# Optimization experiments

Hardware: AMD Instinct MI355X
Metric: run time of the kernel (lower is better)

## Reference

```python
import jax, jax.numpy as jnp
import numpy as np

H, DK, DV = 4, 64, 64        # heads, key/value head dims (hidden=256)
M, TOPK = 4, 2               # num memories, router top-k
GN, EPS, COND_SCALE = 16.0, 1e-5, 1.0


def setup_inputs() -> dict:
    key = jax.random.key(0)
    ks = jax.random.split(key, 12)
    B, Q, K, D = 8, 64, 256, 256
    w = lambda k, shape, fan: jax.random.normal(k, shape, jnp.float32) / np.sqrt(fan).astype(np.float32)
    return {
        "query": jax.random.normal(ks[0], (B, Q, D), jnp.float32),
        "keyval": jax.random.normal(ks[1], (B, K, D), jnp.float32),
        "attention_mask_kv": jnp.ones((B, K), jnp.int32),
        "W_cond": w(ks[2], (D, D), D),
        "W_q": w(ks[3], (D, H * DK), D),
        "W_k": w(ks[4], (D, H * DK), D),
        "W_v": w(ks[5], (D, H * DV), D),
        "W_gk1": w(ks[6], (D, 16), D),
        "W_gk2": w(ks[7], (16, H * DK), 16),
        "b_gk2": jnp.zeros((H * DK,), jnp.float32),
        "W_router": w(ks[8], (D, M), D),
        "norm_w": jnp.ones((DV,), jnp.float32),
        "W_o": w(ks[9], (H * DV, D), H * DV),
    }


def _mem_last(q_last, k, v, gk, sel, wgt):
    """Last-token output of one gated linear-attention memory.
    S_t = diag(exp(gk_t)) S_{t-1} + k_t v_t^T ; o_T = q_T S_T.
    q_last: (N,H,DK); k,gk: (N,K,H,DK); v: (N,K,H,DV); sel,wgt: (N,K)."""
    k_e = k * sel[:, :, None, None]
    v_e = v * wgt[:, :, None, None]
    gk_e = gk * sel[:, :, None, None]          # unselected tokens: no decay, no update
    G = jnp.cumsum(gk_e, axis=1)               # (N,K,H,DK), log decays
    decay = jnp.exp(G[:, -1:, :, :] - G)       # remaining decay to last step, <= 1
    s = jnp.einsum('nhd,nthd->nth', q_last, k_e * decay)
    return jnp.einsum('nth,nthv->nhv', s, v_e)


def reference(query, keyval, attention_mask_kv, W_cond, W_q, W_k, W_v,
              W_gk1, W_gk2, b_gk2, W_router, norm_w, W_o):
    B, Q, D = query.shape
    K = keyval.shape[1]
    N = B * Q
    # broadcast KV expansion + cond injection
    cond = (query @ W_cond) * COND_SCALE                         # (B,Q,D)
    x = (keyval[:, None, :, :] + cond[:, :, None, :]).reshape(N, K, D)
    m = jnp.broadcast_to(attention_mask_kv[:, None, :].astype(x.dtype), (B, Q, K)).reshape(N, K)
    # projections
    q = (x @ W_q).reshape(N, K, H, DK)
    k = (x @ W_k).reshape(N, K, H, DK) * m[:, :, None, None]
    v = (x @ W_v).reshape(N, K, H, DV) * m[:, :, None, None]
    gk = (jax.nn.log_sigmoid(x @ W_gk1 @ W_gk2 + b_gk2) / GN).reshape(N, K, H, DK)
    gk = gk * m[:, :, None, None]
    # router: softmax -> top-k -> renormalize
    router_logits = (x @ W_router).reshape(N * K, M)
    probs = jax.nn.softmax(router_logits, axis=-1)
    topv, topi = jax.lax.top_k(probs, TOPK)
    topv = topv / jnp.sum(topv, axis=-1, keepdims=True)
    w_mem = jnp.sum(jax.nn.one_hot(topi, M, dtype=x.dtype) * topv[..., None], axis=-2)
    w_mem = w_mem.reshape(N, K, M)
    # shared memory (always on) + routed memories
    q_last = q[:, -1]
    ones = jnp.ones((N, K), x.dtype)
    o = _mem_last(q_last, k, v, gk, ones, ones)
    for e in range(M):
        we = w_mem[:, :, e]
        o = o + _mem_last(q_last, k, v, gk, (we > 0).astype(x.dtype), we)
    # per-head RMSNorm + output projection
    o = o * jax.lax.rsqrt(jnp.mean(o * o, axis=-1, keepdims=True) + EPS) * norm_w
    out = (o.reshape(N, H * DV) @ W_o).reshape(B, Q, D)
    return out, router_logits
```

## Files before the change

kernel.cpp:

```cpp
#include <hip/hip_runtime.h>
#include <math.h>

#define Bb   8
#define Qq   64
#define Kk   256
#define Dd   256
#define Nn   (Bb * Qq)
#define GNi  0.0625f
#define EPSf 1e-5f
#define WB   1088

__device__ __forceinline__ float wred(float x) {
#pragma unroll
    for (int off = 32; off > 0; off >>= 1)
        x += __shfl_xor(x, off, 64);
    return x;
}

__global__ __launch_bounds__(256) void pack_wb(
    const float* __restrict__ Wq, const float* __restrict__ Wk,
    const float* __restrict__ Wv, const float* __restrict__ Wg1,
    const float* __restrict__ Wg2, const float* __restrict__ Wr,
    float* __restrict__ Wb)
{
    const int idx = blockIdx.x * 256 + threadIdx.x;
    const int k = idx / WB, j = idx % WB;
    float v;
    if (j < 256)       v = Wq[(size_t)k * 256 + j];
    else if (j < 512)  v = Wk[(size_t)k * 256 + j - 256];
    else if (j < 768)  v = Wv[(size_t)k * 256 + j - 512];
    else if (j < 1024) {
        const int c = j - 768;
        float s = 0.f;
#pragma unroll
        for (int i = 0; i < 16; ++i)
            s = fmaf(Wg1[(size_t)k * 16 + i], Wg2[(size_t)i * 256 + c], s);
        v = s;
    }
    else if (j < 1028) v = Wr[(size_t)k * 4 + (j - 1024)];
    else               v = 0.f;
    Wb[idx] = v;
}

__device__ __forceinline__ void gemm_core(
    const float* __restrict__ A, const float* __restrict__ Bm, int ldb,
    float (&acc)[8][4], float* As, float* Ws)
{
    const int tid = threadIdx.x;
    const int r  = tid >> 1;
    const int kl = (tid & 1) * 8;
    const int wc = tid & 63;
    const int kr = (tid >> 6) * 4;
    const int ty = tid >> 4;
    const int tx = tid & 15;

    for (int k0 = 0; k0 < Dd; k0 += 16) {
        const float4 a0 = *(const float4*)(A + (size_t)r * Dd + k0 + kl);
        const float4 a1 = *(const float4*)(A + (size_t)r * Dd + k0 + kl + 4);
        As[(kl + 0) * 132 + r] = a0.x;
        As[(kl + 1) * 132 + r] = a0.y;
        As[(kl + 2) * 132 + r] = a0.z;
        As[(kl + 3) * 132 + r] = a0.w;
        As[(kl + 4) * 132 + r] = a1.x;
        As[(kl + 5) * 132 + r] = a1.y;
        As[(kl + 6) * 132 + r] = a1.z;
        As[(kl + 7) * 132 + r] = a1.w;
#pragma unroll
        for (int u = 0; u < 4; ++u)
            Ws[(kr + u) * 68 + wc] = Bm[(size_t)(k0 + kr + u) * ldb + wc];
        __syncthreads();
#pragma unroll
        for (int kk = 0; kk < 16; ++kk) {
            const float4 aL = *(const float4*)&As[kk * 132 + ty * 8];
            const float4 aH = *(const float4*)&As[kk * 132 + ty * 8 + 4];
            const float4 bv = *(const float4*)&Ws[kk * 68 + tx * 4];
            const float av[8] = {aL.x, aL.y, aL.z, aL.w, aH.x, aH.y, aH.z, aH.w};
            const float bw[4] = {bv.x, bv.y, bv.z, bv.w};
#pragma unroll
            for (int i = 0; i < 8; ++i)
#pragma unroll
                for (int j = 0; j < 4; ++j)
                    acc[i][j] = fmaf(av[i], bw[j], acc[i][j]);
        }
        __syncthreads();
    }
}

__global__ __launch_bounds__(256) void gemm1(
    const float* __restrict__ keyval, const float* __restrict__ query,
    const float* __restrict__ Wb, const float* __restrict__ W_cond,
    float* __restrict__ KVi, float* __restrict__ KVr,
    float* __restrict__ cond, float* __restrict__ KVq8)
{
    __shared__ float As[16 * 132];
    __shared__ float Ws[16 * 68];
    const int id = blockIdx.x;
    const int tid = threadIdx.x;

    if (id == 224) {
        for (int b8 = 0; b8 < 8; ++b8)
            As[b8 * 256 + tid] = keyval[((size_t)b8 * Kk + 255) * Dd + tid];
        __syncthreads();
        float acc8[8] = {};
        for (int k = 0; k < 256; ++k) {
            const float wq = Wb[(size_t)k * WB + tid];
#pragma unroll
            for (int b8 = 0; b8 < 8; ++b8)
                acc8[b8] = fmaf(As[b8 * 256 + k], wq, acc8[b8]);
        }
        for (int b8 = 0; b8 < 8; ++b8)
            KVq8[b8 * 256 + tid] = acc8[b8];
        return;
    }

    float acc[8][4] = {};
    const int ty = tid >> 4, tx = tid & 15;

    if (id < 208) {
        const int bm  = (id / 13) * 128;
        const int bnA = 256 + (id % 13) * 64;
        gemm_core(keyval + (size_t)bm * Dd, Wb + bnA, WB, acc, As, Ws);
        if (bnA < 1024) {
            const int reg = (bnA >> 8) - 1;
            const int cb  = bnA & 255;
#pragma unroll
            for (int i = 0; i < 8; ++i) {
                const size_t rowo = (size_t)(bm + ty * 8 + i) * 1024;
#pragma unroll
                for (int jj = 0; jj < 4; ++jj)
                    KVi[rowo + (size_t)(cb + tx * 4 + jj) * 4 + reg] = acc[i][jj];
            }
        } else if (tx == 0) {
#pragma unroll
            for (int i = 0; i < 8; ++i)
                *(float4*)&KVr[(size_t)(bm + ty * 8 + i) * 4] =
                    make_float4(acc[i][0], acc[i][1], acc[i][2], acc[i][3]);
        }
    } else {
        const int id2 = id - 208;
        const int bm = (id2 >> 2) * 128;
        const int bn = (id2 & 3) * 64;
        gemm_core(query + (size_t)bm * Dd, W_cond + bn, Dd, acc, As, Ws);
#pragma unroll
        for (int i = 0; i < 8; ++i)
            *(float4*)&cond[(size_t)(bm + ty * 8 + i) * Dd + bn + tx * 4] =
                make_float4(acc[i][0], acc[i][1], acc[i][2], acc[i][3]);
    }
}

__global__ __launch_bounds__(256) void gemm2(
    const float* __restrict__ cond, const float* __restrict__ Wb,
    float* __restrict__ Cbi, float* __restrict__ Cr)
{
    __shared__ float As[16 * 132];
    __shared__ float Ws[16 * 68];
    const int id = blockIdx.x;
    const int tid = threadIdx.x;
    const int bm = (id / 17) * 128;
    const int bn = (id % 17) * 64;
    float acc[8][4] = {};
    gemm_core(cond + (size_t)bm * Dd, Wb + bn, WB, acc, As, Ws);
    const int ty = tid >> 4, tx = tid & 15;
    if (bn < 1024) {
        const int reg = bn >> 8;
        const int cb  = bn & 255;
#pragma unroll
        for (int i = 0; i < 8; ++i) {
            const size_t rowo = (size_t)(bm + ty * 8 + i) * 1024;
#pragma unroll
            for (int jj = 0; jj < 4; ++jj)
                Cbi[rowo + (size_t)(cb + tx * 4 + jj) * 4 + reg] = acc[i][jj];
        }
    } else if (tx == 0) {
#pragma unroll
        for (int i = 0; i < 8; ++i)
            *(float4*)&Cr[(size_t)(bm + ty * 8 + i) * 4] =
                make_float4(acc[i][0], acc[i][1], acc[i][2], acc[i][3]);
    }
}

__device__ __forceinline__ void tile_step(
    const float4* buf, int t0, const int* __restrict__ pm, const float4* wm,
    float ql, float kc, float vc, float pc,
    float& E0, float& E1, float& E2, float& E3, float& E4, float& o,
    float (*Pt)[68], float* sb, int lane, int tl, int qq)
{
    float vreg[16];
#pragma unroll
    for (int i = 0; i < 16; ++i) {
        const int t = t0 + 15 - i;
        const float mf = (float)pm[t];
        const float4 kv = buf[i];
        const float kkv = (kv.x + kc) * mf;
        vreg[i] = (kv.y + vc) * mf;
        const float pre = kv.z + pc;
        const float4 w = wm[t];
        const float ls = fminf(pre, 0.f) - __logf(1.f + __expf(-fabsf(pre)));
        float dg = __expf(ls * GNi);
        dg = (mf != 0.f) ? dg : 1.f;
        const float zf = E0 + w.x * E1 + w.y * E2 + w.z * E3 + w.w * E4;
        Pt[i][lane] = ql * kkv * zf;
        E0 *= dg;
        E1 *= (w.x > 0.f) ? dg : 1.f;
        E2 *= (w.y > 0.f) ? dg : 1.f;
        E3 *= (w.z > 0.f) ? dg : 1.f;
        E4 *= (w.w > 0.f) ? dg : 1.f;
    }
    __builtin_amdgcn_wave_barrier();
    float s = 0.f;
#pragma unroll
    for (int r = 0; r < 4; ++r) {
        const float4 p4 = *(const float4*)&Pt[tl][qq * 16 + r * 4];
        s += (p4.x + p4.y) + (p4.z + p4.w);
    }
    s += __shfl_xor(s, 16, 64);
    s += __shfl_xor(s, 32, 64);
    sb[tl] = s;
    __builtin_amdgcn_wave_barrier();
#pragma unroll
    for (int r = 0; r < 4; ++r) {
        const float4 sv = *(const float4*)&sb[r * 4];
        o = fmaf(sv.x, vreg[r * 4 + 0], o);
        o = fmaf(sv.y, vreg[r * 4 + 1], o);
        o = fmaf(sv.z, vreg[r * 4 + 2], o);
        o = fmaf(sv.w, vreg[r * 4 + 3], o);
    }
}

__global__ __launch_bounds__(256, 2) void mom_fused(
    const float4* __restrict__ KVi, const float* __restrict__ KVr,
    const float4* __restrict__ Cbi, const float* __restrict__ Cr,
    const float* __restrict__ KVq8, const float* __restrict__ b_gk2,
    const int* __restrict__ mask, const float* __restrict__ W_o,
    const float* __restrict__ norm_w,
    float* __restrict__ out, float* __restrict__ logits)
{
    __shared__ float4 wm[Kk];
    __shared__ float  Ptile[4][16][68];
    __shared__ float  sbuf[4][16];
    __shared__ float  onorm[Dd];

    const int n = blockIdx.x;
    const int b = n >> 6;
    const int j = threadIdx.x;
    const int lane = j & 63;
    const int wv = j >> 6;

    const float4 c4 = Cbi[(size_t)n * 256 + j];
    const float qc = c4.x, kc = c4.y, vc = c4.z;
    const float pc = c4.w + b_gk2[j];
    const float ql = KVq8[b * 256 + j] + qc;

    {
        const float4 kvr = *(const float4*)&KVr[(size_t)(b * Kk + j) * 4];
        const float4 cr  = *(const float4*)&Cr[(size_t)n * 4];
        float l[4] = {kvr.x + cr.x, kvr.y + cr.y, kvr.z + cr.z, kvr.w + cr.w};
        *(float4*)(logits + ((size_t)n * Kk + j) * 4) =
            make_float4(l[0], l[1], l[2], l[3]);

        int i1 = 0;
#pragma unroll
        for (int q = 1; q < 4; ++q) if (l[q] > l[i1]) i1 = q;
        int i2 = -1;
#pragma unroll
        for (int q = 0; q < 4; ++q) {
            if (q == i1) continue;
            if (i2 < 0 || l[q] > l[i2]) i2 = q;
        }
        const float mx = fmaxf(l[i1], l[i2]);
        const float e1 = __expf(l[i1] - mx);
        const float e2 = __expf(l[i2] - mx);
        const float inv = 1.f / (e1 + e2);
        float w[4] = {0.f, 0.f, 0.f, 0.f};
        w[i1] = e1 * inv;
        w[i2] = e2 * inv;
        wm[j] = make_float4(w[0], w[1], w[2], w[3]);
    }
    __syncthreads();

    const float4* pkv = KVi + (size_t)b * Kk * 256 + j;
    const int*    pm  = mask + b * Kk;

    float E0 = 1.f, E1 = 1.f, E2 = 1.f, E3 = 1.f, E4 = 1.f;
    float o = 0.f;
    const int tl = lane & 15, qq = lane >> 4;

    float4 bufA[16], bufB[16];
#pragma unroll
    for (int i = 0; i < 16; ++i) bufA[i] = pkv[(size_t)(255 - i) * 256];

    for (int pp = 0; pp < 8; ++pp) {
        const int tA = 240 - 32 * pp;
        const int tB = tA - 16;
#pragma unroll
        for (int i = 0; i < 16; ++i) bufB[i] = pkv[(size_t)(tB + 15 - i) * 256];
        tile_step(bufA, tA, pm, wm, ql, kc, vc, pc,
                  E0, E1, E2, E3, E4, o, Ptile[wv], sbuf[wv], lane, tl, qq);
        if (pp < 7) {
#pragma unroll
            for (int i = 0; i < 16; ++i)
                bufA[i] = pkv[(size_t)(tB - 16 + 15 - i) * 256];
        }
        tile_step(bufB, tB, pm, wm, ql, kc, vc, pc,
                  E0, E1, E2, E3, E4, o, Ptile[wv], sbuf[wv], lane, tl, qq);
    }

    const float ms = wred(o * o) * (1.0f / 64.0f);
    onorm[j] = o * rsqrtf(ms + EPSf) * norm_w[lane];
    __syncthreads();

    float acc = 0.f;
#pragma unroll 8
    for (int k = 0; k < Dd; ++k)
        acc = fmaf(onorm[k], W_o[(size_t)k * Dd + j], acc);
    out[(size_t)n * Dd + j] = acc;
}

extern "C" void kernel_launch(void* const* d_in, const int* in_sizes, int n_in,
                              void* d_out, int out_size, void* d_ws, size_t ws_size,
                              hipStream_t stream)
{
    const float* query    = (const float*)d_in[0];
    const float* keyval   = (const float*)d_in[1];
    const int*   mask     = (const int*)  d_in[2];
    const float* W_cond   = (const float*)d_in[3];
    const float* W_q      = (const float*)d_in[4];
    const float* W_k      = (const float*)d_in[5];
    const float* W_v      = (const float*)d_in[6];
    const float* W_gk1    = (const float*)d_in[7];
    const float* W_gk2    = (const float*)d_in[8];
    const float* b_gk2    = (const float*)d_in[9];
    const float* W_router = (const float*)d_in[10];
    const float* norm_w   = (const float*)d_in[11];
    const float* W_o      = (const float*)d_in[12];

    float* out    = (float*)d_out;
    float* logits = out + Nn * Dd;

    float* p = (float*)d_ws;
    float* Wb   = p; p += Dd * WB;
    float* KVi  = p; p += (size_t)Bb * Kk * 1024;
    float* KVr  = p; p += Bb * Kk * 4;
    float* cond = p; p += Nn * Dd;
    float* Cbi  = p; p += (size_t)Nn * 1024;
    float* Cr   = p; p += Nn * 4;
    float* KVq8 = p; p += Bb * Dd;

    pack_wb<<<(Dd * WB) / 256, dim3(256), 0, stream>>>(
        W_q, W_k, W_v, W_gk1, W_gk2, W_router, Wb);

    gemm1<<<225, dim3(256), 0, stream>>>(
        keyval, query, Wb, W_cond, KVi, KVr, cond, KVq8);

    gemm2<<<68, dim3(256), 0, stream>>>(cond, Wb, Cbi, Cr);

    mom_fused<<<Nn, dim3(256), 0, stream>>>(
        (const float4*)KVi, KVr, (const float4*)Cbi, Cr,
        KVq8, b_gk2, mask, W_o, norm_w, out, logits);
}
```

Before: 208.0 us.

## Restructure projection GEMMs, shrink recurrence tile, swizzle blocks across XCDs

Drops the weight-packing kernel and replaces the two GEMM kernels with a prep kernel and a main GEMM. The main GEMM uses a 64x64 tile with register prefetch, computes several projections against one shared A tile, and writes the interleaved k/v/g layout with float4 stores. The router projections become simple per-element dot products. In the fused recurrence kernel, the time tile shrinks from 16 to 8 steps, the mask is staged in LDS, and the block-to-row mapping is swizzled so each batch's KV data stays on one XCD's L2. The risks are more barrier and reduction rounds per time step and lower reuse in the smaller GEMM tiles.

```diff
diff --git a/kernel.cpp b/kernel.cpp
--- a/kernel.cpp
+++ b/kernel.cpp
@@ -8,7 +8,6 @@
 #define Nn   (Bb * Qq)
 #define GNi  0.0625f
 #define EPSf 1e-5f
-#define WB   1088
 
 __device__ __forceinline__ float wred(float x) {
 #pragma unroll
@@ -17,179 +16,183 @@
     return x;
 }
 
-__global__ __launch_bounds__(256) void pack_wb(
-    const float* __restrict__ Wq, const float* __restrict__ Wk,
-    const float* __restrict__ Wv, const float* __restrict__ Wg1,
+template<int R>
+__device__ __forceinline__ void gemm64(
+    const float* __restrict__ A, int lda,
+    const float* __restrict__ B0, const float* __restrict__ B1,
+    const float* __restrict__ B2, const float* __restrict__ B3,
+    int bn, int Kc, float (&acc)[R][16], float* As, float* Ws)
+{
+    const int tid = threadIdx.x;
+    const int aRow = tid >> 2, aCol = (tid & 3) * 4;
+    const int wr = tid >> 4, wcb = (tid & 15) * 4;
+    const int ty = tid >> 4, tx = tid & 15;
+    const float* Bp[4] = {B0, B1, B2, B3};
+
+    float4 rA = *(const float4*)(A + (size_t)aRow * lda + aCol);
+    float4 rW[R];
+#pragma unroll
+    for (int r = 0; r < R; ++r)
+        rW[r] = *(const float4*)(Bp[r] + (size_t)wr * 256 + bn + wcb);
+
+    for (int k0 = 0; k0 < Kc; k0 += 16) {
+        __syncthreads();
+        As[(aCol + 0) * 68 + aRow] = rA.x;
+        As[(aCol + 1) * 68 + aRow] = rA.y;
+        As[(aCol + 2) * 68 + aRow] = rA.z;
+        As[(aCol + 3) * 68 + aRow] = rA.w;
+#pragma unroll
+        for (int r = 0; r < R; ++r)
+            *(float4*)&Ws[r * 1088 + wr * 68 + wcb] = rW[r];
+        __syncthreads();
+        if (k0 + 16 < Kc) {
+            rA = *(const float4*)(A + (size_t)aRow * lda + k0 + 16 + aCol);
+#pragma unroll
+            for (int r = 0; r < R; ++r)
+                rW[r] = *(const float4*)(Bp[r] + (size_t)(k0 + 16 + wr) * 256 + bn + wcb);
+        }
+#pragma unroll
+        for (int kk = 0; kk < 16; ++kk) {
+            const float4 a4 = *(const float4*)&As[kk * 68 + ty * 4];
+            const float av[4] = {a4.x, a4.y, a4.z, a4.w};
+#pragma unroll
+            for (int r = 0; r < R; ++r) {
+                const float4 b4 = *(const float4*)&Ws[r * 1088 + kk * 68 + tx * 4];
+                const float bw[4] = {b4.x, b4.y, b4.z, b4.w};
+#pragma unroll
+                for (int i = 0; i < 4; ++i)
+#pragma unroll
+                    for (int j = 0; j < 4; ++j)
+                        acc[r][i * 4 + j] = fmaf(av[i], bw[j], acc[r][i * 4 + j]);
+            }
+        }
+    }
+}
+
+__global__ __launch_bounds__(256) void prep(
+    const float* __restrict__ query, const float* __restrict__ keyval,
+    const float* __restrict__ W_cond, const float* __restrict__ Wg1,
     const float* __restrict__ Wg2, const float* __restrict__ Wr,
-    float* __restrict__ Wb)
-{
-    const int idx = blockIdx.x * 256 + threadIdx.x;
-    const int k = idx / WB, j = idx % WB;
-    float v;
-    if (j < 256)       v = Wq[(size_t)k * 256 + j];
-    else if (j < 512)  v = Wk[(size_t)k * 256 + j - 256];
-    else if (j < 768)  v = Wv[(size_t)k * 256 + j - 512];
-    else if (j < 1024) {
-        const int c = j - 768;
-        float s = 0.f;
-#pragma unroll
-        for (int i = 0; i < 16; ++i)
-            s = fmaf(Wg1[(size_t)k * 16 + i], Wg2[(size_t)i * 256 + c], s);
-        v = s;
-    }
-    else if (j < 1028) v = Wr[(size_t)k * 4 + (j - 1024)];
-    else               v = 0.f;
-    Wb[idx] = v;
-}
-
-__device__ __forceinline__ void gemm_core(
-    const float* __restrict__ A, const float* __restrict__ Bm, int ldb,
-    float (&acc)[8][4], float* As, float* Ws)
-{
-    const int tid = threadIdx.x;
-    const int r  = tid >> 1;
-    const int kl = (tid & 1) * 8;
-    const int wc = tid & 63;
-    const int kr = (tid >> 6) * 4;
-    const int ty = tid >> 4;
-    const int tx = tid & 15;
-
-    for (int k0 = 0; k0 < Dd; k0 += 16) {
-        const float4 a0 = *(const float4*)(A + (size_t)r * Dd + k0 + kl);
-        const float4 a1 = *(const float4*)(A + (size_t)r * Dd + k0 + kl + 4);
-        As[(kl + 0) * 132 + r] = a0.x;
-        As[(kl + 1) * 132 + r] = a0.y;
-        As[(kl + 2) * 132 + r] = a0.z;
-        As[(kl + 3) * 132 + r] = a0.w;
-        As[(kl + 4) * 132 + r] = a1.x;
-        As[(kl + 5) * 132 + r] = a1.y;
-        As[(kl + 6) * 132 + r] = a1.z;
-        As[(kl + 7) * 132 + r] = a1.w;
-#pragma unroll
-        for (int u = 0; u < 4; ++u)
-            Ws[(kr + u) * 68 + wc] = Bm[(size_t)(k0 + kr + u) * ldb + wc];
-        __syncthreads();
-#pragma unroll
-        for (int kk = 0; kk < 16; ++kk) {
-            const float4 aL = *(const float4*)&As[kk * 132 + ty * 8];
-            const float4 aH = *(const float4*)&As[kk * 132 + ty * 8 + 4];
-            const float4 bv = *(const float4*)&Ws[kk * 68 + tx * 4];
-            const float av[8] = {aL.x, aL.y, aL.z, aL.w, aH.x, aH.y, aH.z, aH.w};
-            const float bw[4] = {bv.x, bv.y, bv.z, bv.w};
-#pragma unroll
-            for (int i = 0; i < 8; ++i)
-#pragma unroll
-                for (int j = 0; j < 4; ++j)
-                    acc[i][j] = fmaf(av[i], bw[j], acc[i][j]);
-        }
-        __syncthreads();
-    }
-}
-
-__global__ __launch_bounds__(256) void gemm1(
-    const float* __restrict__ keyval, const float* __restrict__ query,
-    const float* __restrict__ Wb, const float* __restrict__ W_cond,
-    float* __restrict__ KVi, float* __restrict__ KVr,
-    float* __restrict__ cond, float* __restrict__ KVq8)
-{
-    __shared__ float As[16 * 132];
-    __shared__ float Ws[16 * 68];
+    const float* __restrict__ Wq,
+    float* __restrict__ cond, float* __restrict__ Wg,
+    float* __restrict__ KVr, float* __restrict__ KVq8)
+{
+    __shared__ float lds[2 * 1088];
     const int id = blockIdx.x;
     const int tid = threadIdx.x;
 
-    if (id == 224) {
+    if (id < 48) {
+        float acc[1][16] = {};
+        const int ty = tid >> 4, tx = tid & 15;
+        if (id < 32) {
+            const int bm = (id >> 2) * 64, bn = (id & 3) * 64;
+            gemm64<1>(query + (size_t)bm * Dd, Dd, W_cond, nullptr, nullptr, nullptr,
+                      bn, Dd, acc, lds, lds + 1088);
+#pragma unroll
+            for (int i = 0; i < 4; ++i)
+                *(float4*)&cond[(size_t)(bm + ty * 4 + i) * Dd + bn + tx * 4] =
+                    make_float4(acc[0][i * 4 + 0], acc[0][i * 4 + 1],
+                                acc[0][i * 4 + 2], acc[0][i * 4 + 3]);
+        } else {
+            const int id3 = id - 32;
+            const int bm = (id3 >> 2) * 64, bn = (id3 & 3) * 64;
+            gemm64<1>(Wg1 + (size_t)bm * 16, 16, Wg2, nullptr, nullptr, nullptr,
+                      bn, 16, acc, lds, lds + 1088);
+#pragma unroll
+            for (int i = 0; i < 4; ++i)
+                *(float4*)&Wg[(size_t)(bm + ty * 4 + i) * Dd + bn + tx * 4] =
+                    make_float4(acc[0][i * 4 + 0], acc[0][i * 4 + 1],
+                                acc[0][i * 4 + 2], acc[0][i * 4 + 3]);
+        }
+        return;
+    }
+    if (id < 80) {
+        const int idx = (id - 48) * 256 + tid;
+        const int row = idx >> 2, col = idx & 3;
+        float a = 0.f;
+        for (int k = 0; k < 256; ++k)
+            a = fmaf(keyval[(size_t)row * Dd + k], Wr[(size_t)k * 4 + col], a);
+        KVr[idx] = a;
+        return;
+    }
+    for (int b8 = 0; b8 < 8; ++b8)
+        lds[b8 * 256 + tid] = keyval[((size_t)b8 * Kk + 255) * Dd + tid];
+    __syncthreads();
+    float a8[8] = {};
+    for (int k = 0; k < 256; ++k) {
+        const float wq = Wq[(size_t)k * Dd + tid];
+#pragma unroll
         for (int b8 = 0; b8 < 8; ++b8)
-            As[b8 * 256 + tid] = keyval[((size_t)b8 * Kk + 255) * Dd + tid];
-        __syncthreads();
-        float acc8[8] = {};
-        for (int k = 0; k < 256; ++k) {
-            const float wq = Wb[(size_t)k * WB + tid];
-#pragma unroll
-            for (int b8 = 0; b8 < 8; ++b8)
-                acc8[b8] = fmaf(As[b8 * 256 + k], wq, acc8[b8]);
-        }
-        for (int b8 = 0; b8 < 8; ++b8)
-            KVq8[b8 * 256 + tid] = acc8[b8];
-        return;
-    }
-
-    float acc[8][4] = {};
-    const int ty = tid >> 4, tx = tid & 15;
-
-    if (id < 208) {
-        const int bm  = (id / 13) * 128;
-        const int bnA = 256 + (id % 13) * 64;
-        gemm_core(keyval + (size_t)bm * Dd, Wb + bnA, WB, acc, As, Ws);
-        if (bnA < 1024) {
-            const int reg = (bnA >> 8) - 1;
-            const int cb  = bnA & 255;
-#pragma unroll
-            for (int i = 0; i < 8; ++i) {
-                const size_t rowo = (size_t)(bm + ty * 8 + i) * 1024;
-#pragma unroll
-                for (int jj = 0; jj < 4; ++jj)
-                    KVi[rowo + (size_t)(cb + tx * 4 + jj) * 4 + reg] = acc[i][jj];
-            }
-        } else if (tx == 0) {
-#pragma unroll
-            for (int i = 0; i < 8; ++i)
-                *(float4*)&KVr[(size_t)(bm + ty * 8 + i) * 4] =
-                    make_float4(acc[i][0], acc[i][1], acc[i][2], acc[i][3]);
-        }
-    } else {
-        const int id2 = id - 208;
-        const int bm = (id2 >> 2) * 128;
-        const int bn = (id2 & 3) * 64;
-        gemm_core(query + (size_t)bm * Dd, W_cond + bn, Dd, acc, As, Ws);
-#pragma unroll
-        for (int i = 0; i < 8; ++i)
-            *(float4*)&cond[(size_t)(bm + ty * 8 + i) * Dd + bn + tx * 4] =
-                make_float4(acc[i][0], acc[i][1], acc[i][2], acc[i][3]);
-    }
-}
-
-__global__ __launch_bounds__(256) void gemm2(
-    const float* __restrict__ cond, const float* __restrict__ Wb,
-    float* __restrict__ Cbi, float* __restrict__ Cr)
-{
-    __shared__ float As[16 * 132];
-    __shared__ float Ws[16 * 68];
+            a8[b8] = fmaf(lds[b8 * 256 + k], wq, a8[b8]);
+    }
+    for (int b8 = 0; b8 < 8; ++b8)
+        KVq8[b8 * 256 + tid] = a8[b8];
+}
+
+__global__ __launch_bounds__(256) void maingemm(
+    const float* __restrict__ keyval, const float* __restrict__ cond,
+    const float* __restrict__ Wq, const float* __restrict__ Wk,
+    const float* __restrict__ Wv, const float* __restrict__ Wg,
+    const float* __restrict__ Wr,
+    float* __restrict__ KVi, float* __restrict__ Cbi, float* __restrict__ Cr)
+{
+    __shared__ float lds[5 * 1088];
     const int id = blockIdx.x;
     const int tid = threadIdx.x;
-    const int bm = (id / 17) * 128;
-    const int bn = (id % 17) * 64;
-    float acc[8][4] = {};
-    gemm_core(cond + (size_t)bm * Dd, Wb + bn, WB, acc, As, Ws);
     const int ty = tid >> 4, tx = tid & 15;
-    if (bn < 1024) {
-        const int reg = bn >> 8;
-        const int cb  = bn & 255;
-#pragma unroll
-        for (int i = 0; i < 8; ++i) {
-            const size_t rowo = (size_t)(bm + ty * 8 + i) * 1024;
-#pragma unroll
-            for (int jj = 0; jj < 4; ++jj)
-                Cbi[rowo + (size_t)(cb + tx * 4 + jj) * 4 + reg] = acc[i][jj];
-        }
-    } else if (tx == 0) {
-#pragma unroll
-        for (int i = 0; i < 8; ++i)
-            *(float4*)&Cr[(size_t)(bm + ty * 8 + i) * 4] =
-                make_float4(acc[i][0], acc[i][1], acc[i][2], acc[i][3]);
-    }
-}
-
-__device__ __forceinline__ void tile_step(
-    const float4* buf, int t0, const int* __restrict__ pm, const float4* wm,
+
+    if (id < 128) {
+        const int bm = (id >> 2) * 64;
+        const int bn = (id & 3) * 64;
+        float acc[3][16] = {};
+        gemm64<3>(keyval + (size_t)bm * Dd, Dd, Wk, Wv, Wg, nullptr,
+                  bn, Dd, acc, lds, lds + 1088);
+#pragma unroll
+        for (int i = 0; i < 4; ++i) {
+            const size_t rowo = (size_t)(bm + ty * 4 + i) * 1024;
+#pragma unroll
+            for (int j = 0; j < 4; ++j)
+                *(float4*)&KVi[rowo + (size_t)(bn + tx * 4 + j) * 4] =
+                    make_float4(acc[0][i * 4 + j], acc[1][i * 4 + j],
+                                acc[2][i * 4 + j], 0.f);
+        }
+    } else if (id < 160) {
+        const int id2 = id - 128;
+        const int bm = (id2 >> 2) * 64;
+        const int bn = (id2 & 3) * 64;
+        float acc[4][16] = {};
+        gemm64<4>(cond + (size_t)bm * Dd, Dd, Wq, Wk, Wv, Wg,
+                  bn, Dd, acc, lds, lds + 1088);
+#pragma unroll
+        for (int i = 0; i < 4; ++i) {
+            const size_t rowo = (size_t)(bm + ty * 4 + i) * 1024;
+#pragma unroll
+            for (int j = 0; j < 4; ++j)
+                *(float4*)&Cbi[rowo + (size_t)(bn + tx * 4 + j) * 4] =
+                    make_float4(acc[0][i * 4 + j], acc[1][i * 4 + j],
+                                acc[2][i * 4 + j], acc[3][i * 4 + j]);
+        }
+    } else {
+        const int idx = (id - 160) * 256 + tid;
+        const int row = idx >> 2, col = idx & 3;
+        float a = 0.f;
+        for (int k = 0; k < 256; ++k)
+            a = fmaf(cond[(size_t)row * Dd + k], Wr[(size_t)k * 4 + col], a);
+        Cr[idx] = a;
+    }
+}
+
+__device__ __forceinline__ void tile_step8(
+    const float4* buf, int thi, const float* mfs, const float4* wm,
     float ql, float kc, float vc, float pc,
     float& E0, float& E1, float& E2, float& E3, float& E4, float& o,
     float (*Pt)[68], float* sb, int lane, int tl, int qq)
 {
-    float vreg[16];
-#pragma unroll
-    for (int i = 0; i < 16; ++i) {
-        const int t = t0 + 15 - i;
-        const float mf = (float)pm[t];
+    float vreg[8];
+#pragma unroll
+    for (int i = 0; i < 8; ++i) {
+        const int t = thi - i;
+        const float mf = mfs[t];
         const float4 kv = buf[i];
         const float kkv = (kv.x + kc) * mf;
         vreg[i] = (kv.y + vc) * mf;
@@ -198,7 +201,7 @@
         const float ls = fminf(pre, 0.f) - __logf(1.f + __expf(-fabsf(pre)));
         float dg = __expf(ls * GNi);
         dg = (mf != 0.f) ? dg : 1.f;
-        const float zf = E0 + w.x * E1 + w.y * E2 + w.z * E3 + w.w * E4;
+        const float zf = (E0 + w.x * E1) + (w.y * E2 + w.z * E3) + w.w * E4;
         Pt[i][lane] = ql * kkv * zf;
         E0 *= dg;
         E1 *= (w.x > 0.f) ? dg : 1.f;
@@ -207,24 +210,20 @@
         E4 *= (w.w > 0.f) ? dg : 1.f;
     }
     __builtin_amdgcn_wave_barrier();
-    float s = 0.f;
-#pragma unroll
-    for (int r = 0; r < 4; ++r) {
-        const float4 p4 = *(const float4*)&Pt[tl][qq * 16 + r * 4];
-        s += (p4.x + p4.y) + (p4.z + p4.w);
-    }
+    const float4 p0 = *(const float4*)&Pt[tl][qq * 8];
+    const float4 p1 = *(const float4*)&Pt[tl][qq * 8 + 4];
+    float s = ((p0.x + p0.y) + (p0.z + p0.w)) + ((p1.x + p1.y) + (p1.z + p1.w));
+    s += __shfl_xor(s, 8, 64);
     s += __shfl_xor(s, 16, 64);
     s += __shfl_xor(s, 32, 64);
     sb[tl] = s;
     __builtin_amdgcn_wave_barrier();
-#pragma unroll
-    for (int r = 0; r < 4; ++r) {
-        const float4 sv = *(const float4*)&sb[r * 4];
-        o = fmaf(sv.x, vreg[r * 4 + 0], o);
-        o = fmaf(sv.y, vreg[r * 4 + 1], o);
-        o = fmaf(sv.z, vreg[r * 4 + 2], o);
-        o = fmaf(sv.w, vreg[r * 4 + 3], o);
-    }
+    const float4 s0 = *(const float4*)&sb[0];
+    const float4 s1 = *(const float4*)&sb[4];
+    o = fmaf(s0.x, vreg[0], o); o = fmaf(s0.y, vreg[1], o);
+    o = fmaf(s0.z, vreg[2], o); o = fmaf(s0.w, vreg[3], o);
+    o = fmaf(s1.x, vreg[4], o); o = fmaf(s1.y, vreg[5], o);
+    o = fmaf(s1.z, vreg[6], o); o = fmaf(s1.w, vreg[7], o);
 }
 
 __global__ __launch_bounds__(256, 2) void mom_fused(
@@ -235,13 +234,15 @@
     const float* __restrict__ norm_w,
     float* __restrict__ out, float* __restrict__ logits)
 {
-    __shared__ float4 wm[Kk];
-    __shared__ float  Ptile[4][16][68];
-    __shared__ float  sbuf[4][16];
-    __shared__ float  onorm[Dd];
-
-    const int n = blockIdx.x;
-    const int b = n >> 6;
+    __shared__ __align__(16) float4 wm[Kk];
+    __shared__ __align__(16) float  mfs[Kk];
+    __shared__ __align__(16) float  Ptile[4][8][68];
+    __shared__ __align__(16) float  sbuf[4][8];
+    __shared__ __align__(16) float  onorm[Dd];
+
+    const int bi = blockIdx.x;
+    const int n = (bi & 7) * 64 + (bi >> 3);
+    const int b = bi & 7;
     const int j = threadIdx.x;
     const int lane = j & 63;
     const int wv = j >> 6;
@@ -252,6 +253,7 @@
     const float ql = KVq8[b * 256 + j] + qc;
 
     {
+        mfs[j] = (float)mask[b * Kk + j];
         const float4 kvr = *(const float4*)&KVr[(size_t)(b * Kk + j) * 4];
         const float4 cr  = *(const float4*)&Cr[(size_t)n * 4];
         float l[4] = {kvr.x + cr.x, kvr.y + cr.y, kvr.z + cr.z, kvr.w + cr.w};
@@ -279,30 +281,28 @@
     __syncthreads();
 
     const float4* pkv = KVi + (size_t)b * Kk * 256 + j;
-    const int*    pm  = mask + b * Kk;
 
     float E0 = 1.f, E1 = 1.f, E2 = 1.f, E3 = 1.f, E4 = 1.f;
     float o = 0.f;
-    const int tl = lane & 15, qq = lane >> 4;
-
-    float4 bufA[16], bufB[16];
-#pragma unroll
-    for (int i = 0; i < 16; ++i) bufA[i] = pkv[(size_t)(255 - i) * 256];
-
-    for (int pp = 0; pp < 8; ++pp) {
-        const int tA = 240 - 32 * pp;
-        const int tB = tA - 16;
-#pragma unroll
-        for (int i = 0; i < 16; ++i) bufB[i] = pkv[(size_t)(tB + 15 - i) * 256];
-        tile_step(bufA, tA, pm, wm, ql, kc, vc, pc,
-                  E0, E1, E2, E3, E4, o, Ptile[wv], sbuf[wv], lane, tl, qq);
-        if (pp < 7) {
-#pragma unroll
-            for (int i = 0; i < 16; ++i)
-                bufA[i] = pkv[(size_t)(tB - 16 + 15 - i) * 256];
-        }
-        tile_step(bufB, tB, pm, wm, ql, kc, vc, pc,
-                  E0, E1, E2, E3, E4, o, Ptile[wv], sbuf[wv], lane, tl, qq);
+    const int tl = lane & 7, qq = lane >> 3;
+
+    float4 bufA[8], bufB[8];
+#pragma unroll
+    for (int i = 0; i < 8; ++i) bufA[i] = pkv[(size_t)(255 - i) * 256];
+
+    for (int p = 0; p < 16; ++p) {
+        const int tA = 255 - 16 * p;
+        const int tB = tA - 8;
+#pragma unroll
+        for (int i = 0; i < 8; ++i) bufB[i] = pkv[(size_t)(tB - i) * 256];
+        tile_step8(bufA, tA, mfs, wm, ql, kc, vc, pc,
+                   E0, E1, E2, E3, E4, o, Ptile[wv], sbuf[wv], lane, tl, qq);
+        if (p < 15) {
+#pragma unroll
+            for (int i = 0; i < 8; ++i) bufA[i] = pkv[(size_t)(tB - 8 - i) * 256];
+        }
+        tile_step8(bufB, tB, mfs, wm, ql, kc, vc, pc,
+                   E0, E1, E2, E3, E4, o, Ptile[wv], sbuf[wv], lane, tl, qq);
     }
 
     const float ms = wred(o * o) * (1.0f / 64.0f);
@@ -338,21 +338,20 @@
     float* logits = out + Nn * Dd;
 
     float* p = (float*)d_ws;
-    float* Wb   = p; p += Dd * WB;
+    float* Wg   = p; p += Dd * Dd;
+    float* cond = p; p += Nn * Dd;
     float* KVi  = p; p += (size_t)Bb * Kk * 1024;
     float* KVr  = p; p += Bb * Kk * 4;
-    float* cond = p; p += Nn * Dd;
     float* Cbi  = p; p += (size_t)Nn * 1024;
     float* Cr   = p; p += Nn * 4;
     float* KVq8 = p; p += Bb * Dd;
 
-    pack_wb<<<(Dd * WB) / 256, dim3(256), 0, stream>>>(
-        W_q, W_k, W_v, W_gk1, W_gk2, W_router, Wb);
-
-    gemm1<<<225, dim3(256), 0, stream>>>(
-        keyval, query, Wb, W_cond, KVi, KVr, cond, KVq8);
-
-    gemm2<<<68, dim3(256), 0, stream>>>(cond, Wb, Cbi, Cr);
+    prep<<<81, dim3(256), 0, stream>>>(
+        query, keyval, W_cond, W_gk1, W_gk2, W_router, W_q,
+        cond, Wg, KVr, KVq8);
+
+    maingemm<<<168, dim3(256), 0, stream>>>(
+        keyval, cond, W_q, W_k, W_v, Wg, W_router, KVi, Cbi, Cr);
 
     mom_fused<<<Nn, dim3(256), 0, stream>>>(
         (const float4*)KVi, KVr, (const float4*)Cbi, Cr,
```

After: 212.2 us. 1.02x slower.
